# Kernel tuning notes

Hardware: AMD Instinct MI355X
Metric: run time of the kernel (lower is better)

The kernel has to match this reference:

```python
import jax, jax.numpy as jnp
import numpy as np
import math

B, S, E, H, L, F, V, MAXLEN = 2, 1024, 1024, 16, 6, 4096, 400, 1024
DH = E // H
PAD_ID = 0


def setup_inputs() -> dict:
    key = jax.random.key(0)
    ks = jax.random.split(key, 12)
    nrm = lambda k, shape, s=0.02: jax.random.normal(k, shape, jnp.float32) * s
    inp = {}
    inp["sequences"] = jax.random.randint(ks[0], (B, S), 3, V + 3)
    inp["map1"] = jax.random.randint(ks[1], (V + 3,), 0, V + 3)
    inp["map2"] = jax.random.randint(ks[2], (V + 3,), 0, V + 3)
    inp["emb"] = nrm(ks[3], (V + 3, E), 1.0)          # nn.Embedding N(0,1)
    inp["pos_emb"] = nrm(ks[4], (MAXLEN + 2, E), 1.0)  # learned positional (torch.randn)
    inp["dist_emb"] = nrm(ks[5], (MAXLEN + 1, H), 0.02)
    inp["in_proj_w"] = nrm(ks[6], (L, 3 * E, E))
    inp["in_proj_b"] = jnp.zeros((L, 3 * E), jnp.float32)
    inp["out_proj_w"] = nrm(ks[7], (L, E, E))
    inp["out_proj_b"] = jnp.zeros((L, E), jnp.float32)
    inp["lin1_w"] = nrm(ks[8], (L, F, E))
    inp["lin1_b"] = jnp.zeros((L, F), jnp.float32)
    inp["lin2_w"] = nrm(ks[9], (L, E, F))
    inp["lin2_b"] = jnp.zeros((L, E), jnp.float32)
    inp["ln1_w"] = jnp.ones((L, E), jnp.float32)
    inp["ln1_b"] = jnp.zeros((L, E), jnp.float32)
    inp["ln2_w"] = jnp.ones((L, E), jnp.float32)
    inp["ln2_b"] = jnp.zeros((L, E), jnp.float32)
    inp["fnorm_w"] = jnp.ones((E,), jnp.float32)
    inp["fnorm_b"] = jnp.zeros((E,), jnp.float32)
    inp["gen_w"] = nrm(ks[10], (V, E))
    inp["gen_b"] = jnp.zeros((V,), jnp.float32)
    return inp


def _layer_norm(x, w, b, eps=1e-5):
    m = x.mean(-1, keepdims=True)
    v = x.var(-1, keepdims=True)
    return (x - m) * jax.lax.rsqrt(v + eps) * w + b


def reference(sequences, map1, map2, emb, pos_emb, dist_emb,
              in_proj_w, in_proj_b, out_proj_w, out_proj_b,
              lin1_w, lin1_b, lin2_w, lin2_b,
              ln1_w, ln1_b, ln2_w, ln2_b,
              fnorm_w, fnorm_b, gen_w, gen_b):
    Bv, Sv = sequences.shape
    # TokenEmbedding: average of two node embeddings, scaled by sqrt(E), + learned pos
    x = (jnp.take(emb, map1[sequences], axis=0) +
         jnp.take(emb, map2[sequences], axis=0)) * (math.sqrt(E) / 2.0)
    x = x + pos_emb[:Sv]  # broadcast over batch
    # Learned relative-position bias + causal mask + key padding
    idx = jnp.arange(Sv)
    dist = jnp.minimum(jnp.abs(idx[None, :] - idx[:, None]), MAXLEN)
    bias = jnp.take(dist_emb, dist, axis=0).transpose(2, 0, 1)  # [H,S,S]
    causal = idx[None, :] <= idx[:, None]                        # key j <= query i
    neg_inf = jnp.float32(-jnp.inf)
    mask = jnp.where(causal[None], bias, neg_inf)                # [H,S,S]
    pad = sequences == PAD_ID                                    # [B,S]
    mask = jnp.where(pad[:, None, None, :], neg_inf, mask[None]) # [B,H,S,S]
    scale = 1.0 / math.sqrt(DH)
    for i in range(L):  # post-norm TransformerEncoderLayer, gelu
        qkv = x @ in_proj_w[i].T + in_proj_b[i]
        q, k, v = jnp.split(qkv, 3, axis=-1)
        q = q.reshape(Bv, Sv, H, DH)
        k = k.reshape(Bv, Sv, H, DH)
        v = v.reshape(Bv, Sv, H, DH)
        scores = jnp.einsum('bihd,bjhd->bhij', q, k) * scale + mask
        attn = jax.nn.softmax(scores, axis=-1)
        ctx = jnp.einsum('bhij,bjhd->bihd', attn, v).reshape(Bv, Sv, E)
        a = ctx @ out_proj_w[i].T + out_proj_b[i]
        x = _layer_norm(x + a, ln1_w[i], ln1_b[i])
        h = jax.nn.gelu(x @ lin1_w[i].T + lin1_b[i], approximate=False)
        ff = h @ lin2_w[i].T + lin2_b[i]
        x = _layer_norm(x + ff, ln2_w[i], ln2_b[i])
    x = _layer_norm(x, fnorm_w, fnorm_b)
    return x @ gen_w.T + gen_b  # [B,S,V]
```

## Files before the change

### kernel.cpp

```cpp
#include <hip/hip_runtime.h>
#include <hip/hip_bf16.h>
#include <math.h>


#define BB 2
#define SS 1024
#define EE 1024
#define HH 16
#define LL 6
#define FF 4096
#define VV 400
#define DH 64
#define STR 68

typedef float f32x4 __attribute__((ext_vector_type(4)));
typedef __bf16 bf16x8 __attribute__((ext_vector_type(8)));

__global__ __launch_bounds__(256) void embed_kernel(
    const int* __restrict__ seq, const int* __restrict__ map1,
    const int* __restrict__ map2, const float* __restrict__ emb,
    const float* __restrict__ pos, float* __restrict__ x)
{
    const int bid = blockIdx.x;
    const int sIdx = bid & (SS - 1);
    const int t = threadIdx.x;
    const int tok = seq[bid];
    const int i1 = map1[tok], i2 = map2[tok];
#pragma unroll
    for (int c = 0; c < 4; ++c) {
        int e = t + c * 256;
        float val = (emb[(size_t)i1 * EE + e] + emb[(size_t)i2 * EE + e]) * 16.0f
                  + pos[(size_t)sIdx * EE + e];
        x[(size_t)bid * EE + e] = val;
    }
}

template <int ACT>
__global__ __launch_bounds__(256) void gemm_nt(
    const float* __restrict__ A, const float* __restrict__ W,
    const float* __restrict__ bias, float* __restrict__ C,
    int M, int N, int K)
{
    __shared__ __align__(16) float As[16][68];
    __shared__ __align__(16) float Wsh[16][68];
    const int t = threadIdx.x;
    const int tx = t & 15, ty = t >> 4;
    const int mBase = blockIdx.y * 64, nBase = blockIdx.x * 64;
    const int lr = t >> 2;
    const int lk = (t & 3) << 2;
    float acc[4][4] = {};
    const float* aPtr = A + (size_t)(mBase + lr) * K + lk;
    const int n = nBase + lr;
    const float* wPtr = W + (size_t)n * K + lk;

    for (int k0 = 0; k0 < K; k0 += 16) {
        float4 av = *(const float4*)(aPtr + k0);
        As[lk + 0][lr] = av.x; As[lk + 1][lr] = av.y;
        As[lk + 2][lr] = av.z; As[lk + 3][lr] = av.w;
        float4 wv = make_float4(0.f, 0.f, 0.f, 0.f);
        if (n < N) wv = *(const float4*)(wPtr + k0);
        Wsh[lk + 0][lr] = wv.x; Wsh[lk + 1][lr] = wv.y;
        Wsh[lk + 2][lr] = wv.z; Wsh[lk + 3][lr] = wv.w;
        __syncthreads();
#pragma unroll
        for (int kk = 0; kk < 16; ++kk) {
            const float4 a = *(const float4*)&As[kk][ty * 4];
            const float4 w = *(const float4*)&Wsh[kk][tx * 4];
            acc[0][0] += a.x * w.x; acc[0][1] += a.x * w.y; acc[0][2] += a.x * w.z; acc[0][3] += a.x * w.w;
            acc[1][0] += a.y * w.x; acc[1][1] += a.y * w.y; acc[1][2] += a.y * w.z; acc[1][3] += a.y * w.w;
            acc[2][0] += a.z * w.x; acc[2][1] += a.z * w.y; acc[2][2] += a.z * w.z; acc[2][3] += a.z * w.w;
            acc[3][0] += a.w * w.x; acc[3][1] += a.w * w.y; acc[3][2] += a.w * w.z; acc[3][3] += a.w * w.w;
        }
        __syncthreads();
    }
#pragma unroll
    for (int i = 0; i < 4; ++i) {
        const int m = mBase + ty * 4 + i;
#pragma unroll
        for (int j = 0; j < 4; ++j) {
            const int nn = nBase + tx * 4 + j;
            if (nn < N) {
                float v = acc[i][j] + bias[nn];
                if (ACT == 1) v = 0.5f * v * (1.0f + erff(v * 0.70710678118654752f));
                C[(size_t)m * N + nn] = v;
            }
        }
    }
}

__device__ __forceinline__ void split_frag(const f32x4 f0, const f32x4 f1,
                                           bf16x8& h, bf16x8& l)
{
#pragma unroll
    for (int i = 0; i < 4; ++i) {
        float a = f0[i];
        __bf16 ha = (__bf16)a;
        h[i] = ha;
        l[i] = (__bf16)(a - (float)ha);
        float b = f1[i];
        __bf16 hb = (__bf16)b;
        h[i + 4] = hb;
        l[i + 4] = (__bf16)(b - (float)hb);
    }
}

template <int BM, int BN, int WM, int WN, int ACT>
__global__ __launch_bounds__(256) void gemm_mfma(
    const float* __restrict__ A, const float* __restrict__ W,
    const float* __restrict__ bias, float* __restrict__ C,
    int M, int N, int K)
{
    constexpr int BK = 32;
    constexpr int MF = WM / 16;
    constexpr int NF = WN / 16;
    constexpr int WAVES_N = BN / WN;
    constexpr int TILE = (BM + BN) * BK;
    constexpr int LOADS = BM / 32 + BN / 32;
    static_assert((BM / WM) * WAVES_N == 4, "4 waves per block");

    __shared__ __align__(16) float smem[2 * TILE];

    const int t = threadIdx.x;
    const int wave = t >> 6;
    const int lane = t & 63;
    const int wr = wave / WAVES_N;
    const int wc = wave % WAVES_N;
    const int mBase = blockIdx.y * BM;
    const int nBase = blockIdx.x * BN;

    const int srow = lane >> 3;
    const int schunk = (lane & 7) ^ srow;
    const float* aSrc = A + (size_t)(mBase + srow) * K + schunk * 4;
    const float* wSrc = W + (size_t)(nBase + srow) * K + schunk * 4;

    f32x4 acc[MF][NF];
    const f32x4 zed = {0.f, 0.f, 0.f, 0.f};
#pragma unroll
    for (int i = 0; i < MF; ++i)
#pragma unroll
        for (int j = 0; j < NF; ++j) acc[i][j] = zed;

    const int frow = lane & 15;
    const int c0 = (lane >> 4) << 1;

#define STAGE(bufptr, k0)                                                     \
    {                                                                          \
        float* As_ = (bufptr);                                                 \
        float* Ws_ = (bufptr) + BM * BK;                                       \
        _Pragma("unroll")                                                      \
        for (int i = 0; i < BM / 32; ++i)                                      \
            __builtin_amdgcn_global_load_lds(                                  \
                (const __attribute__((address_space(1))) void*)                \
                    (aSrc + (size_t)(i * 32 + wave * 8) * K + (k0)),           \
                (__attribute__((address_space(3))) void*)                      \
                    ((char*)As_ + (i * 4 + wave) * 1024), 16, 0, 0);           \
        _Pragma("unroll")                                                      \
        for (int i = 0; i < BN / 32; ++i)                                      \
            __builtin_amdgcn_global_load_lds(                                  \
                (const __attribute__((address_space(1))) void*)                \
                    (wSrc + (size_t)(i * 32 + wave * 8) * K + (k0)),           \
                (__attribute__((address_space(3))) void*)                      \
                    ((char*)Ws_ + (i * 4 + wave) * 1024), 16, 0, 0);           \
    }

#define COMPUTE(bufptr)                                                        \
    {                                                                          \
        const float* As_ = (bufptr);                                           \
        const float* Ws_ = (bufptr) + BM * BK;                                 \
        bf16x8 ah[MF], al[MF], bh[NF], bl[NF];                                 \
        _Pragma("unroll")                                                      \
        for (int i = 0; i < MF; ++i) {                                         \
            const int r = wr * WM + i * 16 + frow;                             \
            const int s = r & 7;                                               \
            const float* base = As_ + r * BK;                                  \
            f32x4 f0 = *(const f32x4*)(base + ((c0 ^ s) << 2));                \
            f32x4 f1 = *(const f32x4*)(base + (((c0 + 1) ^ s) << 2));          \
            split_frag(f0, f1, ah[i], al[i]);                                  \
        }                                                                      \
        _Pragma("unroll")                                                      \
        for (int j = 0; j < NF; ++j) {                                         \
            const int r = wc * WN + j * 16 + frow;                             \
            const int s = r & 7;                                               \
            const float* base = Ws_ + r * BK;                                  \
            f32x4 f0 = *(const f32x4*)(base + ((c0 ^ s) << 2));                \
            f32x4 f1 = *(const f32x4*)(base + (((c0 + 1) ^ s) << 2));          \
            split_frag(f0, f1, bh[j], bl[j]);                                  \
        }                                                                      \
        _Pragma("unroll")                                                      \
        for (int i = 0; i < MF; ++i)                                           \
            _Pragma("unroll")                                                  \
            for (int j = 0; j < NF; ++j) {                                     \
                acc[i][j] = __builtin_amdgcn_mfma_f32_16x16x32_bf16(ah[i], bh[j], acc[i][j], 0, 0, 0); \
                acc[i][j] = __builtin_amdgcn_mfma_f32_16x16x32_bf16(ah[i], bl[j], acc[i][j], 0, 0, 0); \
                acc[i][j] = __builtin_amdgcn_mfma_f32_16x16x32_bf16(al[i], bh[j], acc[i][j], 0, 0, 0); \
            }                                                                  \
    }

    const int NT = K / BK;
    STAGE(smem, 0);
    int cur = 0;
    for (int tt = 0; tt < NT - 1; ++tt) {
        float* curBuf = smem + cur * TILE;
        float* nxtBuf = smem + (cur ^ 1) * TILE;
        STAGE(nxtBuf, (tt + 1) * BK);
        asm volatile("s_waitcnt vmcnt(%0)" :: "n"(LOADS) : "memory");
        __builtin_amdgcn_s_barrier();
        COMPUTE(curBuf);
        asm volatile("s_waitcnt lgkmcnt(0)" ::: "memory");
        __builtin_amdgcn_s_barrier();
        cur ^= 1;
    }
    {
        float* curBuf = smem + cur * TILE;
        asm volatile("s_waitcnt vmcnt(0)" ::: "memory");
        __builtin_amdgcn_s_barrier();
        COMPUTE(curBuf);
    }
#undef STAGE
#undef COMPUTE

    const int crow = (lane >> 4) << 2;
    const int ccol = lane & 15;
#pragma unroll
    for (int i = 0; i < MF; ++i) {
        const int row = mBase + wr * WM + i * 16 + crow;
#pragma unroll
        for (int j = 0; j < NF; ++j) {
            const int col = nBase + wc * WN + j * 16 + ccol;
            const float bv = bias[col];
            float* cp = C + (size_t)row * N + col;
#pragma unroll
            for (int r = 0; r < 4; ++r) {
                float v = acc[i][j][r] + bv;
                if (ACT == 1) v = 0.5f * v * (1.0f + erff(v * 0.70710678118654752f));
                cp[(size_t)r * N] = v;
            }
        }
    }
}

__global__ __launch_bounds__(256) void fattn_kernel(
    const float* __restrict__ qkv, const float* __restrict__ dist_emb,
    float* __restrict__ ctx)
{
    __shared__ __align__(16) float Qs[64][STR];
    __shared__ __align__(16) float Ks[64][STR];
    __shared__ __align__(16) float Vs[64][STR];
    __shared__ __align__(16) float Ps[64][STR];
    __shared__ float bias_l[1024];
    __shared__ float redm[4][64];
    __shared__ float reds[4][64];
    __shared__ float mstate[64], lstate[64], alphas[64];

    const int t = threadIdx.x;
    const int tx = t & 15, ty = t >> 4;
    const int bid = blockIdx.x;
    const int qt = bid & 15;
    const int h  = (bid >> 4) & (HH - 1);
    const int b  = bid >> 8;
    const int i0 = qt * 64;

    for (int d = t; d < 1024; d += 256) bias_l[d] = dist_emb[d * HH + h];
    if (t < 64) { mstate[t] = -INFINITY; lstate[t] = 0.f; }

    {
        const int colb = tx * 4;
#pragma unroll
        for (int c = 0; c < 4; ++c) {
            const int row = (t >> 4) + 16 * c;
            float4 qv = *(const float4*)(qkv + (size_t)(b * SS + i0 + row) * (3 * EE) + h * DH + colb);
            Qs[colb + 0][row] = qv.x; Qs[colb + 1][row] = qv.y;
            Qs[colb + 2][row] = qv.z; Qs[colb + 3][row] = qv.w;
        }
    }

    float O[4][4] = {};
    const int q = t & 63, part = t >> 6;
    const int iQ = i0 + q;

    for (int kt = 0; kt <= qt; ++kt) {
        const int j0 = kt * 64;
        __syncthreads();
        {
            const int colb = tx * 4;
#pragma unroll
            for (int c = 0; c < 4; ++c) {
                const int row = (t >> 4) + 16 * c;
                const float* base = qkv + (size_t)(b * SS + j0 + row) * (3 * EE) + h * DH + colb;
                float4 kv = *(const float4*)(base + EE);
                Ks[colb + 0][row] = kv.x; Ks[colb + 1][row] = kv.y;
                Ks[colb + 2][row] = kv.z; Ks[colb + 3][row] = kv.w;
                float4 vv = *(const float4*)(base + 2 * EE);
                *(float4*)&Vs[row][colb] = vv;
            }
        }
        __syncthreads();
        float acc[4][4] = {};
#pragma unroll
        for (int kk = 0; kk < 64; ++kk) {
            const float4 a = *(const float4*)&Qs[kk][ty * 4];
            const float4 w = *(const float4*)&Ks[kk][tx * 4];
            acc[0][0] += a.x * w.x; acc[0][1] += a.x * w.y; acc[0][2] += a.x * w.z; acc[0][3] += a.x * w.w;
            acc[1][0] += a.y * w.x; acc[1][1] += a.y * w.y; acc[1][2] += a.y * w.z; acc[1][3] += a.y * w.w;
            acc[2][0] += a.z * w.x; acc[2][1] += a.z * w.y; acc[2][2] += a.z * w.z; acc[2][3] += a.z * w.w;
            acc[3][0] += a.w * w.x; acc[3][1] += a.w * w.y; acc[3][2] += a.w * w.z; acc[3][3] += a.w * w.w;
        }
#pragma unroll
        for (int j = 0; j < 4; ++j) {
            *(float4*)&Ps[tx * 4 + j][ty * 4] =
                make_float4(acc[0][j], acc[1][j], acc[2][j], acc[3][j]);
        }
        __syncthreads();
        float s[16];
        float mp = -INFINITY;
#pragma unroll
        for (int kk = 0; kk < 16; ++kk) {
            const int k = part * 16 + kk;
            const int j = j0 + k;
            float v;
            if (j > iQ) v = -INFINITY;
            else        v = Ps[k][q] * 0.125f + bias_l[iQ - j];
            s[kk] = v;
            mp = fmaxf(mp, v);
        }
        redm[part][q] = mp;
        __syncthreads();
        const float mtile = fmaxf(fmaxf(redm[0][q], redm[1][q]), fmaxf(redm[2][q], redm[3][q]));
        const float mold = mstate[q];
        const float mnew = fmaxf(mold, mtile);
        const float alpha = __expf(mold - mnew);
        float sum = 0.f;
#pragma unroll
        for (int kk = 0; kk < 16; ++kk) {
            const float p = __expf(s[kk] - mnew);
            Ps[part * 16 + kk][q] = p;
            sum += p;
        }
        reds[part][q] = sum;
        __syncthreads();
        if (part == 0) {
            mstate[q] = mnew;
            lstate[q] = lstate[q] * alpha + reds[0][q] + reds[1][q] + reds[2][q] + reds[3][q];
            alphas[q] = alpha;
        }
        __syncthreads();
        float al[4];
#pragma unroll
        for (int i = 0; i < 4; ++i) al[i] = alphas[ty * 4 + i];
#pragma unroll
        for (int i = 0; i < 4; ++i)
#pragma unroll
            for (int j = 0; j < 4; ++j) O[i][j] *= al[i];
#pragma unroll
        for (int kk = 0; kk < 64; ++kk) {
            const float4 p = *(const float4*)&Ps[kk][ty * 4];
            const float4 v = *(const float4*)&Vs[kk][tx * 4];
            O[0][0] += p.x * v.x; O[0][1] += p.x * v.y; O[0][2] += p.x * v.z; O[0][3] += p.x * v.w;
            O[1][0] += p.y * v.x; O[1][1] += p.y * v.y; O[1][2] += p.y * v.z; O[1][3] += p.y * v.w;
            O[2][0] += p.z * v.x; O[2][1] += p.z * v.y; O[2][2] += p.z * v.z; O[2][3] += p.z * v.w;
            O[3][0] += p.w * v.x; O[3][1] += p.w * v.y; O[3][2] += p.w * v.z; O[3][3] += p.w * v.w;
        }
    }
#pragma unroll
    for (int i = 0; i < 4; ++i) {
        const float linv = 1.0f / lstate[ty * 4 + i];
        const size_t row = (size_t)(b * SS + i0 + ty * 4 + i) * EE + h * DH + tx * 4;
#pragma unroll
        for (int j = 0; j < 4; ++j) ctx[row + j] = O[i][j] * linv;
    }
}

__global__ __launch_bounds__(256) void add_ln_kernel(
    float* __restrict__ x, const float* __restrict__ a,
    const float* __restrict__ w, const float* __restrict__ bb, int hasAdd)
{
    __shared__ float red[8];
    const int row = blockIdx.x, t = threadIdx.x;
    float v[4]; float s = 0.f, ss = 0.f;
#pragma unroll
    for (int c = 0; c < 4; ++c) {
        int e = t + c * 256;
        float val = x[(size_t)row * EE + e];
        if (hasAdd) val += a[(size_t)row * EE + e];
        v[c] = val; s += val; ss += val * val;
    }
#pragma unroll
    for (int o = 32; o > 0; o >>= 1) { s += __shfl_down(s, o); ss += __shfl_down(ss, o); }
    if ((t & 63) == 0) { red[t >> 6] = s; red[4 + (t >> 6)] = ss; }
    __syncthreads();
    s  = red[0] + red[1] + red[2] + red[3];
    ss = red[4] + red[5] + red[6] + red[7];
    const float mean = s * (1.0f / EE);
    const float var  = ss * (1.0f / EE) - mean * mean;
    const float inv  = rsqrtf(var + 1e-5f);
#pragma unroll
    for (int c = 0; c < 4; ++c) {
        int e = t + c * 256;
        x[(size_t)row * EE + e] = (v[c] - mean) * inv * w[e] + bb[e];
    }
}

extern "C" void kernel_launch(void* const* d_in, const int* in_sizes, int n_in,
                              void* d_out, int out_size, void* d_ws, size_t ws_size,
                              hipStream_t stream)
{
    const int*   seq       = (const int*)d_in[0];
    const int*   map1      = (const int*)d_in[1];
    const int*   map2      = (const int*)d_in[2];
    const float* emb       = (const float*)d_in[3];
    const float* pos_emb   = (const float*)d_in[4];
    const float* dist_emb  = (const float*)d_in[5];
    const float* in_proj_w = (const float*)d_in[6];
    const float* in_proj_b = (const float*)d_in[7];
    const float* out_proj_w= (const float*)d_in[8];
    const float* out_proj_b= (const float*)d_in[9];
    const float* lin1_w    = (const float*)d_in[10];
    const float* lin1_b    = (const float*)d_in[11];
    const float* lin2_w    = (const float*)d_in[12];
    const float* lin2_b    = (const float*)d_in[13];
    const float* ln1_w     = (const float*)d_in[14];
    const float* ln1_b     = (const float*)d_in[15];
    const float* ln2_w     = (const float*)d_in[16];
    const float* ln2_b     = (const float*)d_in[17];
    const float* fnorm_w   = (const float*)d_in[18];
    const float* fnorm_b   = (const float*)d_in[19];
    const float* gen_w     = (const float*)d_in[20];
    const float* gen_b     = (const float*)d_in[21];

    float* ws   = (float*)d_ws;
    float* x    = ws;
    float* qkv  = ws + 2097152;
    float* ctx  = ws + 8388608;
    float* t2   = ws + 10485760;
    float* hbuf = ws + 12582912;

    const int M = BB * SS;
    dim3 blk(256);

    embed_kernel<<<M, blk, 0, stream>>>(seq, map1, map2, emb, pos_emb, x);

    for (int l = 0; l < LL; ++l) {
        gemm_mfma<64, 128, 32, 64, 0><<<dim3((3 * EE) / 128, M / 64), blk, 0, stream>>>(
            x, in_proj_w + (size_t)l * 3 * EE * EE, in_proj_b + (size_t)l * 3 * EE,
            qkv, M, 3 * EE, EE);
        fattn_kernel<<<BB * HH * (SS / 64), blk, 0, stream>>>(qkv, dist_emb, ctx);
        gemm_mfma<64, 128, 32, 64, 0><<<dim3(EE / 128, M / 64), blk, 0, stream>>>(
            ctx, out_proj_w + (size_t)l * EE * EE, out_proj_b + (size_t)l * EE,
            t2, M, EE, EE);
        add_ln_kernel<<<M, blk, 0, stream>>>(x, t2, ln1_w + (size_t)l * EE, ln1_b + (size_t)l * EE, 1);
        gemm_mfma<128, 128, 64, 64, 1><<<dim3(FF / 128, M / 128), blk, 0, stream>>>(
            x, lin1_w + (size_t)l * FF * EE, lin1_b + (size_t)l * FF,
            hbuf, M, FF, EE);
        gemm_mfma<64, 128, 32, 64, 0><<<dim3(EE / 128, M / 64), blk, 0, stream>>>(
            hbuf, lin2_w + (size_t)l * EE * FF, lin2_b + (size_t)l * EE,
            t2, M, EE, FF);
        add_ln_kernel<<<M, blk, 0, stream>>>(x, t2, ln2_w + (size_t)l * EE, ln2_b + (size_t)l * EE, 1);
    }
    add_ln_kernel<<<M, blk, 0, stream>>>(x, nullptr, fnorm_w, fnorm_b, 0);
    gemm_nt<0><<<dim3((VV + 63) / 64, M / 64), blk, 0, stream>>>(
        x, gen_w, gen_b, (float*)d_out, M, VV, EE);
}
```

Measured before the change: 2.843 ms.

## Rewrite flash attention with split-bf16 MFMA and register-prefetched K/V tiles

Replaces the scalar-FMA flash attention kernel with one that computes QK^T and PV using bf16 MFMA instructions, keeping fp32-like accuracy by splitting each operand into high and low bf16 parts (three MFMAs per product). Softmax statistics now live in registers and are reduced with wave shuffles rather than through shared memory and extra barriers. The next K/V tile is prefetched into registers while the current one is being processed, V is stored transposed with an XOR swizzle to cut bank conflicts, and query tiles are reversed for odd batches to balance causal work. This trades more instructions for the split-precision emulation and greater register pressure.

```diff
diff --git a/kernel.cpp b/kernel.cpp
--- a/kernel.cpp
+++ b/kernel.cpp
@@ -15,6 +15,30 @@
 
 typedef float f32x4 __attribute__((ext_vector_type(4)));
 typedef __bf16 bf16x8 __attribute__((ext_vector_type(8)));
+typedef unsigned u32x4 __attribute__((ext_vector_type(4)));
+
+__device__ __forceinline__ unsigned short bf16_bits(float f) {
+    union { __bf16 b; unsigned short s; } c; c.b = (__bf16)f; return c.s;
+}
+__device__ __forceinline__ __bf16 bits_bf16(unsigned short s) {
+    union { unsigned short s; __bf16 b; } c; c.s = s; return c.b;
+}
+
+__device__ __forceinline__ void split_frag(const f32x4 f0, const f32x4 f1,
+                                           bf16x8& h, bf16x8& l)
+{
+#pragma unroll
+    for (int i = 0; i < 4; ++i) {
+        float a = f0[i];
+        __bf16 ha = (__bf16)a;
+        h[i] = ha;
+        l[i] = (__bf16)(a - (float)ha);
+        float b = f1[i];
+        __bf16 hb = (__bf16)b;
+        h[i + 4] = hb;
+        l[i + 4] = (__bf16)(b - (float)hb);
+    }
+}
 
 __global__ __launch_bounds__(256) void embed_kernel(
     const int* __restrict__ seq, const int* __restrict__ map1,
@@ -85,22 +109,6 @@
                 C[(size_t)m * N + nn] = v;
             }
         }
-    }
-}
-
-__device__ __forceinline__ void split_frag(const f32x4 f0, const f32x4 f1,
-                                           bf16x8& h, bf16x8& l)
-{
-#pragma unroll
-    for (int i = 0; i < 4; ++i) {
-        float a = f0[i];
-        __bf16 ha = (__bf16)a;
-        h[i] = ha;
-        l[i] = (__bf16)(a - (float)ha);
-        float b = f1[i];
-        __bf16 hb = (__bf16)b;
-        h[i + 4] = hb;
-        l[i + 4] = (__bf16)(b - (float)hb);
     }
 }
 
@@ -239,134 +247,191 @@
     }
 }
 
-__global__ __launch_bounds__(256) void fattn_kernel(
+__global__ __launch_bounds__(256) void fattn_mfma(
     const float* __restrict__ qkv, const float* __restrict__ dist_emb,
     float* __restrict__ ctx)
 {
-    __shared__ __align__(16) float Qs[64][STR];
-    __shared__ __align__(16) float Ks[64][STR];
-    __shared__ __align__(16) float Vs[64][STR];
-    __shared__ __align__(16) float Ps[64][STR];
+    __shared__ __align__(16) float Ks[64][68];
+    __shared__ __align__(16) float Vt[64][68];
+    __shared__ __align__(16) unsigned PsHL[4][16][68];
     __shared__ float bias_l[1024];
-    __shared__ float redm[4][64];
-    __shared__ float reds[4][64];
-    __shared__ float mstate[64], lstate[64], alphas[64];
 
     const int t = threadIdx.x;
-    const int tx = t & 15, ty = t >> 4;
+    const int wave = t >> 6, lane = t & 63;
+    const int x = lane & 15, g = lane >> 4;
     const int bid = blockIdx.x;
-    const int qt = bid & 15;
+    const int b  = bid >> 8;
     const int h  = (bid >> 4) & (HH - 1);
-    const int b  = bid >> 8;
+    int qt = bid & 15;
+    if (b & 1) qt = 15 - qt;
     const int i0 = qt * 64;
 
     for (int d = t; d < 1024; d += 256) bias_l[d] = dist_emb[d * HH + h];
-    if (t < 64) { mstate[t] = -INFINITY; lstate[t] = 0.f; }
-
+
+    bf16x8 qh[2], ql[2];
     {
-        const int colb = tx * 4;
+        const float* qp = qkv + (size_t)(b * SS + i0 + wave * 16 + x) * (3 * EE)
+                          + h * DH + g * 8;
+        f32x4 a0 = *(const f32x4*)qp;
+        f32x4 a1 = *(const f32x4*)(qp + 4);
+        split_frag(a0, a1, qh[0], ql[0]);
+        f32x4 b0 = *(const f32x4*)(qp + 32);
+        f32x4 b1 = *(const f32x4*)(qp + 36);
+        split_frag(b0, b1, qh[1], ql[1]);
+    }
+
+    const f32x4 zed = {0.f, 0.f, 0.f, 0.f};
+    f32x4 O[4] = {zed, zed, zed, zed};
+    float m_reg[4] = {-INFINITY, -INFINITY, -INFINITY, -INFINITY};
+    float l_reg[4] = {0.f, 0.f, 0.f, 0.f};
+
+    const int krow0 = t >> 4;
+    const int kch   = (t & 15) * 4;
+    const int vd    = t & 63;
+    const int sV    = (vd ^ (vd >> 3)) & 7;
+
+    float4 kreg[4], vreg[4];
+#define LOAD_TILE(j0_)                                                         \
+    {                                                                          \
+        _Pragma("unroll")                                                      \
+        for (int c = 0; c < 4; ++c) {                                          \
+            const int row = krow0 + 16 * c;                                    \
+            kreg[c] = *(const float4*)(qkv + (size_t)(b * SS + (j0_) + row) * (3 * EE) \
+                                       + EE + h * DH + kch);                   \
+            const int rc = (t >> 6) + 4 * c;                                   \
+            const float* vb = qkv + (size_t)(b * SS + (j0_) + rc * 4) * (3 * EE) \
+                              + 2 * EE + h * DH + vd;                          \
+            vreg[c].x = vb[0];                                                 \
+            vreg[c].y = vb[3 * EE];                                            \
+            vreg[c].z = vb[6 * EE];                                            \
+            vreg[c].w = vb[9 * EE];                                            \
+        }                                                                      \
+    }
+
+    LOAD_TILE(0);
+
+    for (int kt = 0; kt <= qt; ++kt) {
+        __syncthreads();
 #pragma unroll
         for (int c = 0; c < 4; ++c) {
-            const int row = (t >> 4) + 16 * c;
-            float4 qv = *(const float4*)(qkv + (size_t)(b * SS + i0 + row) * (3 * EE) + h * DH + colb);
-            Qs[colb + 0][row] = qv.x; Qs[colb + 1][row] = qv.y;
-            Qs[colb + 2][row] = qv.z; Qs[colb + 3][row] = qv.w;
-        }
-    }
-
-    float O[4][4] = {};
-    const int q = t & 63, part = t >> 6;
-    const int iQ = i0 + q;
-
-    for (int kt = 0; kt <= qt; ++kt) {
+            *(float4*)&Ks[krow0 + 16 * c][kch] = kreg[c];
+            const int rc = (t >> 6) + 4 * c;
+            *(float4*)&Vt[vd][(rc ^ sV) * 4] = vreg[c];
+        }
+        __syncthreads();
+        if (kt < qt) LOAD_TILE((kt + 1) * 64);
+
+        f32x4 sacc[4] = {zed, zed, zed, zed};
+#pragma unroll
+        for (int ks = 0; ks < 2; ++ks) {
+#pragma unroll
+            for (int j = 0; j < 4; ++j) {
+                const int r = j * 16 + x;
+                f32x4 f0 = *(const f32x4*)&Ks[r][ks * 32 + g * 8];
+                f32x4 f1 = *(const f32x4*)&Ks[r][ks * 32 + g * 8 + 4];
+                bf16x8 kh, kl;
+                split_frag(f0, f1, kh, kl);
+                sacc[j] = __builtin_amdgcn_mfma_f32_16x16x32_bf16(qh[ks], kh, sacc[j], 0, 0, 0);
+                sacc[j] = __builtin_amdgcn_mfma_f32_16x16x32_bf16(qh[ks], kl, sacc[j], 0, 0, 0);
+                sacc[j] = __builtin_amdgcn_mfma_f32_16x16x32_bf16(ql[ks], kh, sacc[j], 0, 0, 0);
+            }
+        }
+
         const int j0 = kt * 64;
-        __syncthreads();
-        {
-            const int colb = tx * 4;
-#pragma unroll
-            for (int c = 0; c < 4; ++c) {
-                const int row = (t >> 4) + 16 * c;
-                const float* base = qkv + (size_t)(b * SS + j0 + row) * (3 * EE) + h * DH + colb;
-                float4 kv = *(const float4*)(base + EE);
-                Ks[colb + 0][row] = kv.x; Ks[colb + 1][row] = kv.y;
-                Ks[colb + 2][row] = kv.z; Ks[colb + 3][row] = kv.w;
-                float4 vv = *(const float4*)(base + 2 * EE);
-                *(float4*)&Vs[row][colb] = vv;
-            }
-        }
-        __syncthreads();
-        float acc[4][4] = {};
-#pragma unroll
-        for (int kk = 0; kk < 64; ++kk) {
-            const float4 a = *(const float4*)&Qs[kk][ty * 4];
-            const float4 w = *(const float4*)&Ks[kk][tx * 4];
-            acc[0][0] += a.x * w.x; acc[0][1] += a.x * w.y; acc[0][2] += a.x * w.z; acc[0][3] += a.x * w.w;
-            acc[1][0] += a.y * w.x; acc[1][1] += a.y * w.y; acc[1][2] += a.y * w.z; acc[1][3] += a.y * w.w;
-            acc[2][0] += a.z * w.x; acc[2][1] += a.z * w.y; acc[2][2] += a.z * w.z; acc[2][3] += a.z * w.w;
-            acc[3][0] += a.w * w.x; acc[3][1] += a.w * w.y; acc[3][2] += a.w * w.z; acc[3][3] += a.w * w.w;
-        }
+        const int qrow = i0 + wave * 16 + g * 4;
+        float pv[4][4], mt[4];
+#pragma unroll
+        for (int r = 0; r < 4; ++r) mt[r] = -INFINITY;
 #pragma unroll
         for (int j = 0; j < 4; ++j) {
-            *(float4*)&Ps[tx * 4 + j][ty * 4] =
-                make_float4(acc[0][j], acc[1][j], acc[2][j], acc[3][j]);
-        }
-        __syncthreads();
-        float s[16];
-        float mp = -INFINITY;
-#pragma unroll
-        for (int kk = 0; kk < 16; ++kk) {
-            const int k = part * 16 + kk;
-            const int j = j0 + k;
-            float v;
-            if (j > iQ) v = -INFINITY;
-            else        v = Ps[k][q] * 0.125f + bias_l[iQ - j];
-            s[kk] = v;
-            mp = fmaxf(mp, v);
-        }
-        redm[part][q] = mp;
-        __syncthreads();
-        const float mtile = fmaxf(fmaxf(redm[0][q], redm[1][q]), fmaxf(redm[2][q], redm[3][q]));
-        const float mold = mstate[q];
-        const float mnew = fmaxf(mold, mtile);
-        const float alpha = __expf(mold - mnew);
-        float sum = 0.f;
-#pragma unroll
-        for (int kk = 0; kk < 16; ++kk) {
-            const float p = __expf(s[kk] - mnew);
-            Ps[part * 16 + kk][q] = p;
-            sum += p;
-        }
-        reds[part][q] = sum;
-        __syncthreads();
-        if (part == 0) {
-            mstate[q] = mnew;
-            lstate[q] = lstate[q] * alpha + reds[0][q] + reds[1][q] + reds[2][q] + reds[3][q];
-            alphas[q] = alpha;
-        }
-        __syncthreads();
-        float al[4];
-#pragma unroll
-        for (int i = 0; i < 4; ++i) al[i] = alphas[ty * 4 + i];
-#pragma unroll
-        for (int i = 0; i < 4; ++i)
-#pragma unroll
-            for (int j = 0; j < 4; ++j) O[i][j] *= al[i];
-#pragma unroll
-        for (int kk = 0; kk < 64; ++kk) {
-            const float4 p = *(const float4*)&Ps[kk][ty * 4];
-            const float4 v = *(const float4*)&Vs[kk][tx * 4];
-            O[0][0] += p.x * v.x; O[0][1] += p.x * v.y; O[0][2] += p.x * v.z; O[0][3] += p.x * v.w;
-            O[1][0] += p.y * v.x; O[1][1] += p.y * v.y; O[1][2] += p.y * v.z; O[1][3] += p.y * v.w;
-            O[2][0] += p.z * v.x; O[2][1] += p.z * v.y; O[2][2] += p.z * v.z; O[2][3] += p.z * v.w;
-            O[3][0] += p.w * v.x; O[3][1] += p.w * v.y; O[3][2] += p.w * v.z; O[3][3] += p.w * v.w;
-        }
-    }
-#pragma unroll
-    for (int i = 0; i < 4; ++i) {
-        const float linv = 1.0f / lstate[ty * 4 + i];
-        const size_t row = (size_t)(b * SS + i0 + ty * 4 + i) * EE + h * DH + tx * 4;
-#pragma unroll
-        for (int j = 0; j < 4; ++j) ctx[row + j] = O[i][j] * linv;
+            const int jg = j0 + j * 16 + x;
+#pragma unroll
+            for (int r = 0; r < 4; ++r) {
+                const int dd = qrow + r - jg;
+                float v = (dd < 0) ? -INFINITY
+                                   : sacc[j][r] * 0.125f + bias_l[dd];
+                pv[j][r] = v;
+                mt[r] = fmaxf(mt[r], v);
+            }
+        }
+#pragma unroll
+        for (int r = 0; r < 4; ++r)
+#pragma unroll
+            for (int msk = 1; msk <= 8; msk <<= 1)
+                mt[r] = fmaxf(mt[r], __shfl_xor(mt[r], msk));
+        float alpha[4], lsum[4];
+#pragma unroll
+        for (int r = 0; r < 4; ++r) {
+            const float mnew = fmaxf(m_reg[r], mt[r]);
+            alpha[r] = __expf(m_reg[r] - mnew);
+            m_reg[r] = mnew;
+            lsum[r] = 0.f;
+        }
+#pragma unroll
+        for (int j = 0; j < 4; ++j)
+#pragma unroll
+            for (int r = 0; r < 4; ++r) {
+                float p = __expf(pv[j][r] - m_reg[r]);
+                pv[j][r] = p;
+                lsum[r] += p;
+            }
+#pragma unroll
+        for (int r = 0; r < 4; ++r) {
+#pragma unroll
+            for (int msk = 1; msk <= 8; msk <<= 1)
+                lsum[r] += __shfl_xor(lsum[r], msk);
+            l_reg[r] = l_reg[r] * alpha[r] + lsum[r];
+            O[0][r] *= alpha[r]; O[1][r] *= alpha[r];
+            O[2][r] *= alpha[r]; O[3][r] *= alpha[r];
+        }
+
+#pragma unroll
+        for (int j = 0; j < 4; ++j)
+#pragma unroll
+            for (int r = 0; r < 4; ++r) {
+                float p = pv[j][r];
+                unsigned short hs = bf16_bits(p);
+                unsigned short ls = bf16_bits(p - (float)bits_bf16(hs));
+                PsHL[wave][g * 4 + r][j * 16 + x] = (unsigned)hs | ((unsigned)ls << 16);
+            }
+
+#pragma unroll
+        for (int ks = 0; ks < 2; ++ks) {
+            const unsigned* pp = &PsHL[wave][x][ks * 32 + g * 8];
+            u32x4 pa = *(const u32x4*)pp;
+            u32x4 pb = *(const u32x4*)(pp + 4);
+            bf16x8 ph, pl;
+#pragma unroll
+            for (int i2 = 0; i2 < 4; ++i2) {
+                ph[i2] = bits_bf16((unsigned short)(pa[i2] & 0xffff));
+                pl[i2] = bits_bf16((unsigned short)(pa[i2] >> 16));
+                ph[i2 + 4] = bits_bf16((unsigned short)(pb[i2] & 0xffff));
+                pl[i2 + 4] = bits_bf16((unsigned short)(pb[i2] >> 16));
+            }
+#pragma unroll
+            for (int j = 0; j < 4; ++j) {
+                const int d = j * 16 + x;
+                const int sv = (d ^ (d >> 3)) & 7;
+                const int c0 = ks * 8 + g * 2;
+                f32x4 f0 = *(const f32x4*)&Vt[d][(c0 ^ sv) * 4];
+                f32x4 f1 = *(const f32x4*)&Vt[d][((c0 + 1) ^ sv) * 4];
+                bf16x8 vh, vl;
+                split_frag(f0, f1, vh, vl);
+                O[j] = __builtin_amdgcn_mfma_f32_16x16x32_bf16(ph, vh, O[j], 0, 0, 0);
+                O[j] = __builtin_amdgcn_mfma_f32_16x16x32_bf16(ph, vl, O[j], 0, 0, 0);
+                O[j] = __builtin_amdgcn_mfma_f32_16x16x32_bf16(pl, vh, O[j], 0, 0, 0);
+            }
+        }
+    }
+#undef LOAD_TILE
+
+#pragma unroll
+    for (int r = 0; r < 4; ++r) {
+        const float linv = 1.0f / l_reg[r];
+        float* cp = ctx + (size_t)(b * SS + i0 + wave * 16 + g * 4 + r) * EE
+                    + h * DH + x;
+#pragma unroll
+        for (int j = 0; j < 4; ++j) cp[j * 16] = O[j][r] * linv;
     }
 }
 
@@ -443,7 +508,7 @@
         gemm_mfma<64, 128, 32, 64, 0><<<dim3((3 * EE) / 128, M / 64), blk, 0, stream>>>(
             x, in_proj_w + (size_t)l * 3 * EE * EE, in_proj_b + (size_t)l * 3 * EE,
             qkv, M, 3 * EE, EE);
-        fattn_kernel<<<BB * HH * (SS / 64), blk, 0, stream>>>(qkv, dist_emb, ctx);
+        fattn_mfma<<<BB * HH * (SS / 64), blk, 0, stream>>>(qkv, dist_emb, ctx);
         gemm_mfma<64, 128, 32, 64, 0><<<dim3(EE / 128, M / 64), blk, 0, stream>>>(
             ctx, out_proj_w + (size_t)l * EE * EE, out_proj_b + (size_t)l * EE,
             t2, M, EE, EE);
```

Result: faster. 2.434 ms (-14.4%).
